# Kernel optimization log

Measured on AMD Instinct MI355X. Metric: run time of the kernel, lower is better.

## Reference

```python
import jax, jax.numpy as jnp
import numpy as np

NUM_CODES = 4096
TEMPERATURE = 1.0
EPS = 1e-08


def setup_inputs() -> dict:
    key = jax.random.key(0)
    k1, k2, k3 = jax.random.split(key, 3)
    B, D, T = 16, 512, 1500
    encoder_stride = 320
    student_features = jax.random.normal(k1, (B, D, T), dtype=jnp.float32)
    codebook = jax.random.normal(k2, (NUM_CODES, D), dtype=jnp.float32)
    lengths = jax.random.randint(k3, (B,), 0, T * encoder_stride, dtype=jnp.int64)
    return {
        "student_features": student_features,
        "codebook": codebook,
        "lengths": lengths,
        "encoder_stride": encoder_stride,
    }


def _length_mask(lengths, T, stride):
    # frame t is valid iff t < floor(length / stride)  -> (B, T) float mask
    n_valid = jnp.minimum(lengths // stride, T)
    return (jnp.arange(T)[None, :] < n_valid[:, None]).astype(jnp.float32)


def reference(student_features, codebook, lengths, encoder_stride):
    B, D, T = student_features.shape
    mask = _length_mask(lengths, T, encoder_stride)            # (B, T)
    z = jnp.transpose(student_features, (0, 2, 1)).reshape(-1, D)  # (N, D), N = B*T
    # Euclidean cdist via ||z||^2 + ||c||^2 - 2 z c^T (same as torch.cdist GEMM path)
    z2 = jnp.sum(z * z, axis=-1, keepdims=True)                # (N, 1)
    c2 = jnp.sum(codebook * codebook, axis=-1)                 # (K,)
    d2 = z2 + c2[None, :] - 2.0 * (z @ codebook.T)             # (N, K)
    distances = jnp.sqrt(jnp.maximum(d2, 1e-12))
    logits = -distances / TEMPERATURE
    probs = jax.nn.softmax(logits, axis=-1)                    # (N, K)
    probs_masked = probs * mask.reshape(-1, 1)
    code_dist = jnp.sum(probs_masked, axis=0)                  # (K,)
    code_dist = code_dist / (jnp.sum(code_dist) + EPS)
    entropy = -jnp.sum(code_dist * jnp.log(code_dist + EPS))
    max_entropy = jnp.log(jnp.float32(NUM_CODES))
    return 1.0 - entropy / max_entropy
```

## Files before the change

### kernel.cpp

```cpp
#include <hip/hip_runtime.h>
#include <hip/hip_bf16.h>

#define NUM_B   16
#define DIM     512
#define TT      1500
#define NROWS   (NUM_B * TT)
#define NCODES  4096
#define ROW_TILES ((NROWS + 127) / 128)
#define NROWS_PAD (ROW_TILES * 128)
#define NSLICE  8
#define SHIFTC  30.0f
#define NBLKX   (NCODES / 128)
#define TBLKS   (NUM_B * 47)
#define CBLKS   (NCODES / 4)
#define NZERO   (NROWS_PAD + NSLICE * NCODES)
#define NZERO2  (NZERO + 1)

typedef __bf16 bf16x8 __attribute__((ext_vector_type(8)));
typedef float  floatx4 __attribute__((ext_vector_type(4)));
typedef unsigned short ushortx8 __attribute__((ext_vector_type(8)));

__device__ __forceinline__ void glds16(const void* g, void* l) {
    __builtin_amdgcn_global_load_lds(
        (__attribute__((address_space(1))) void*)(void*)g,
        (__attribute__((address_space(3))) void*)l, 16, 0, 0);
}

__global__ __launch_bounds__(256) void k_prep(
    const float* __restrict__ sf, const float* __restrict__ cb,
    unsigned short* __restrict__ zbf, unsigned short* __restrict__ cbbf,
    float* __restrict__ z2, float* __restrict__ c2, float* __restrict__ zero0,
    float* __restrict__ outp) {
    int id = blockIdx.x, tid = threadIdx.x;
    if (id < TBLKS) {
        __shared__ float tile[32][257];
        int b = id / 47, t0 = (id % 47) * 32;
        int tl = tid & 31, dg = tid >> 5;
        int tr = tid >> 3, dgr = tid & 7;
        int tg = t0 + tr;
        float ssq = 0.f;
        unsigned short* dst = zbf + (size_t)(b * TT + tg) * DIM;
#pragma unroll
        for (int half = 0; half < 2; ++half) {
            int dbase = half * 256;
            if (half) __syncthreads();
            int t = t0 + tl;
            if (t < TT) {
                const float* src = sf + (size_t)(b * DIM + dbase + dg * 32) * TT + t;
#pragma unroll
                for (int k = 0; k < 32; ++k)
                    tile[tl][dg * 32 + k] = src[(size_t)k * TT];
            }
            __syncthreads();
            if (tg < TT) {
#pragma unroll
                for (int seg = 0; seg < 4; ++seg) {
                    int d0 = seg * 64 + dgr * 8;
                    unsigned int h[8];
#pragma unroll
                    for (int i2 = 0; i2 < 8; ++i2) {
                        __hip_bfloat16 hb = __float2bfloat16(tile[tr][d0 + i2]);
                        h[i2] = __builtin_bit_cast(unsigned short, hb);
                        float vb = __bfloat162float(hb);
                        ssq += vb * vb;
                    }
                    uint4 o;
                    o.x = h[0] | (h[1] << 16); o.y = h[2] | (h[3] << 16);
                    o.z = h[4] | (h[5] << 16); o.w = h[6] | (h[7] << 16);
                    *(uint4*)(dst + dbase + d0) = o;
                }
            }
        }
        ssq += __shfl_xor(ssq, 1); ssq += __shfl_xor(ssq, 2); ssq += __shfl_xor(ssq, 4);
        if (dgr == 0 && tg < TT) z2[b * TT + tg] = ssq;
    } else {
        int ci = id - TBLKS;
        int gid = ci * 256 + tid;
        if (gid < NZERO2) zero0[gid] = 0.f;
        if (ci == 0 && tid == 0) outp[0] = 1.0f;
        int k = ci * 4 + (tid >> 6);
        int lane = tid & 63;
        const float4* src = (const float4*)(cb + (size_t)k * DIM + lane * 8);
        float4 a = src[0], b2 = src[1];
        float vals[8] = {a.x, a.y, a.z, a.w, b2.x, b2.y, b2.z, b2.w};
        float s = 0.f;
        unsigned int h[8];
#pragma unroll
        for (int i = 0; i < 8; ++i) {
            __hip_bfloat16 hb = __float2bfloat16(vals[i]);
            h[i] = __builtin_bit_cast(unsigned short, hb);
            float vb = __bfloat162float(hb);
            s += vb * vb;
        }
        uint4 o;
        o.x = h[0] | (h[1] << 16); o.y = h[2] | (h[3] << 16);
        o.z = h[4] | (h[5] << 16); o.w = h[6] | (h[7] << 16);
        *(uint4*)(cbbf + (size_t)k * DIM + lane * 8) = o;
#pragma unroll
        for (int off = 32; off >= 1; off >>= 1) s += __shfl_down(s, off);
        if (lane == 0) c2[k] = s;
    }
}

__global__ __launch_bounds__(256, 2) void k_gemm1(
    const unsigned short* __restrict__ zbf, const unsigned short* __restrict__ cbbf,
    const float* __restrict__ z2, const float* __restrict__ c2,
    const int* __restrict__ lengths, const int* __restrict__ stride_p,
    float* __restrict__ Sg, unsigned short* __restrict__ Eg) {
    __shared__ unsigned short As[128 * 64];
    __shared__ unsigned short Bs[128 * 64];
    __shared__ float z2s[128], c2s[128];
    __shared__ unsigned char vldp[128];
    __shared__ int s_any;
    int tid = threadIdx.x;
    int r0 = blockIdx.y * 128, c0 = blockIdx.x * 128;
    if (tid == 0) s_any = 0;
    __syncthreads();
    if (tid < 128) {
        int n = r0 + tid;
        int valid = 0;
        if (n < NROWS) {
            int b = n / TT, t = n - b * TT;
            int stride = stride_p[0];
            int nv = lengths[b] / stride;
            if (nv > TT) nv = TT;
            valid = (t < nv);
        }
        if (valid) atomicOr(&s_any, 1);
        vldp[tid] = (unsigned char)valid;
        z2s[tid] = z2[r0 + tid];
        c2s[tid] = c2[c0 + tid];
    }
    __syncthreads();
    if (!s_any) return;

    int wave = tid >> 6, lane = tid & 63;
    int l15 = lane & 15, l4 = lane >> 4;
    int wr = (wave >> 1) * 64, wc = (wave & 1) * 64;

    int srow = lane >> 3;
    int scg = (lane & 7) ^ srow;
    const unsigned short* ag = zbf + (size_t)(r0 + wave * 32 + srow) * DIM + scg * 8;
    const unsigned short* bg = cbbf + (size_t)(c0 + wave * 32 + srow) * DIM + scg * 8;
    unsigned short* al = As + (wave * 32) * 64;
    unsigned short* bl = Bs + (wave * 32) * 64;

    floatx4 acc[4][4];
    const floatx4 zero = {0.f, 0.f, 0.f, 0.f};
#pragma unroll
    for (int i = 0; i < 4; ++i)
#pragma unroll
        for (int j = 0; j < 4; ++j) acc[i][j] = zero;

    int sw = l15 & 7;

    for (int kc = 0; kc < 8; ++kc) {
#pragma unroll
        for (int q = 0; q < 4; ++q) {
            glds16(ag + (size_t)q * 8 * DIM + kc * 64, al + q * 8 * 64);
            glds16(bg + (size_t)q * 8 * DIM + kc * 64, bl + q * 8 * 64);
        }
        __syncthreads();
#pragma unroll
        for (int ks = 0; ks < 64; ks += 32) {
            int g = (ks >> 3) + l4;
            int pcg = g ^ sw;
            bf16x8 av[4], bv[4];
#pragma unroll
            for (int i = 0; i < 4; ++i)
                av[i] = __builtin_bit_cast(bf16x8,
                    *(const ushortx8*)&As[(wr + 16 * i + l15) * 64 + pcg * 8]);
#pragma unroll
            for (int j = 0; j < 4; ++j)
                bv[j] = __builtin_bit_cast(bf16x8,
                    *(const ushortx8*)&Bs[(wc + 16 * j + l15) * 64 + pcg * 8]);
#pragma unroll
            for (int i = 0; i < 4; ++i)
#pragma unroll
                for (int j = 0; j < 4; ++j)
                    acc[i][j] = __builtin_amdgcn_mfma_f32_16x16x32_bf16(bv[j], av[i], acc[i][j], 0, 0, 0);
        }
        __syncthreads();
    }

    float c2r[4][4];
#pragma unroll
    for (int j = 0; j < 4; ++j)
#pragma unroll
        for (int r = 0; r < 4; ++r)
            c2r[j][r] = c2s[wc + 16 * j + 4 * l4 + r];

#pragma unroll
    for (int i = 0; i < 4; ++i) {
        int rl = wr + 16 * i + l15;
        bool rv = vldp[rl] != 0;
        float z2v = z2s[rl];
        float s = 0.f;
        unsigned short* Ep = Eg + (size_t)(r0 + rl) * NCODES + c0 + wc + l4 * 4;
#pragma unroll
        for (int j = 0; j < 4; ++j) {
            float e[4];
#pragma unroll
            for (int r = 0; r < 4; ++r) {
                float d2 = z2v + c2r[j][r] - 2.0f * acc[i][j][r];
                float d = sqrtf(fmaxf(d2, 1e-12f));
                e[r] = __expf(SHIFTC - d);
                s += e[r];
            }
            if (rv) {
                unsigned h0 = __builtin_bit_cast(unsigned short, __float2bfloat16(e[0]));
                unsigned h1 = __builtin_bit_cast(unsigned short, __float2bfloat16(e[1]));
                unsigned h2 = __builtin_bit_cast(unsigned short, __float2bfloat16(e[2]));
                unsigned h3 = __builtin_bit_cast(unsigned short, __float2bfloat16(e[3]));
                uint2 o;
                o.x = h0 | (h1 << 16);
                o.y = h2 | (h3 << 16);
                *(uint2*)(Ep + 16 * j) = o;
            }
        }
        s += __shfl_xor(s, 16); s += __shfl_xor(s, 32);
        if (l4 == 0 && rv) atomicAdd(&Sg[r0 + rl], s);
    }
}

__global__ __launch_bounds__(256) void k_scan(
    const unsigned short* __restrict__ Eg, const float* __restrict__ Sg,
    const int* __restrict__ lengths, const int* __restrict__ stride_p,
    float* __restrict__ cdp) {
    __shared__ float rs2[64];
    __shared__ unsigned char vrows[64];
    __shared__ int s_cnt;
    int tid = threadIdx.x;
    int r0 = blockIdx.y * 64;
    if (tid < 64) {
        int valid = 0;
        float inv = 0.f;
        int n = r0 + tid;
        if (n < NROWS) {
            int b = n / TT, t = n - b * TT;
            int nv = lengths[b] / stride_p[0];
            if (nv > TT) nv = TT;
            valid = (t < nv);
            if (valid) inv = 1.0f / Sg[n];
        }
        unsigned long long mask = __ballot(valid);
        if (tid == 0) s_cnt = __popcll(mask);
        if (valid) {
            int pos = __popcll(mask & ((1ull << tid) - 1ull));
            vrows[pos] = (unsigned char)tid;
            rs2[pos] = inv;
        }
    }
    __syncthreads();
    int m = s_cnt;
    if (m == 0) return;

    int col0 = blockIdx.x * 2048 + tid * 8;
    const unsigned short* base = Eg + (size_t)r0 * NCODES + col0;
    float acc[8] = {0.f, 0.f, 0.f, 0.f, 0.f, 0.f, 0.f, 0.f};

#define ACC8(V, RN) do { \
    unsigned int _u[4] = {(V).x, (V).y, (V).z, (V).w}; \
    _Pragma("unroll") \
    for (int q = 0; q < 4; ++q) { \
        acc[2 * q]     += (RN) * __builtin_bit_cast(float, _u[q] << 16); \
        acc[2 * q + 1] += (RN) * __builtin_bit_cast(float, _u[q] & 0xffff0000u); \
    } \
} while (0)

    int i = 0;
    for (; i + 8 <= m; i += 8) {
        uint4 v0 = *(const uint4*)(base + (size_t)vrows[i]     * NCODES);
        uint4 v1 = *(const uint4*)(base + (size_t)vrows[i + 1] * NCODES);
        uint4 v2 = *(const uint4*)(base + (size_t)vrows[i + 2] * NCODES);
        uint4 v3 = *(const uint4*)(base + (size_t)vrows[i + 3] * NCODES);
        uint4 v4 = *(const uint4*)(base + (size_t)vrows[i + 4] * NCODES);
        uint4 v5 = *(const uint4*)(base + (size_t)vrows[i + 5] * NCODES);
        uint4 v6 = *(const uint4*)(base + (size_t)vrows[i + 6] * NCODES);
        uint4 v7 = *(const uint4*)(base + (size_t)vrows[i + 7] * NCODES);
        ACC8(v0, rs2[i]);     ACC8(v1, rs2[i + 1]);
        ACC8(v2, rs2[i + 2]); ACC8(v3, rs2[i + 3]);
        ACC8(v4, rs2[i + 4]); ACC8(v5, rs2[i + 5]);
        ACC8(v6, rs2[i + 6]); ACC8(v7, rs2[i + 7]);
    }
    for (; i < m; ++i) {
        uint4 v = *(const uint4*)(base + (size_t)vrows[i] * NCODES);
        ACC8(v, rs2[i]);
    }
#undef ACC8

    float* outp = cdp + (size_t)(blockIdx.y & (NSLICE - 1)) * NCODES;
#pragma unroll
    for (int t = 0; t < 8; ++t) atomicAdd(&outp[col0 + t], acc[t]);
}

template <int PASS>
__global__ __launch_bounds__(256, 2) void k_gemm(
    const unsigned short* __restrict__ zbf, const unsigned short* __restrict__ cbbf,
    const float* __restrict__ z2, const float* __restrict__ c2,
    const int* __restrict__ lengths, const int* __restrict__ stride_p,
    float* __restrict__ Sg, float* __restrict__ cd) {
    __shared__ unsigned short Asf[128 * 64];
    __shared__ unsigned short Bsf[128 * 64];
    __shared__ float z2s[128], c2s[128], rs[128];
    __shared__ int s_any;
    int tid = threadIdx.x;
    int r0 = blockIdx.y * 128, c0 = blockIdx.x * 128;
    if (tid == 0) s_any = 0;
    __syncthreads();
    if (tid < 128) {
        int n = r0 + tid;
        int valid = 0;
        if (n < NROWS) {
            int b = n / TT, t = n - b * TT;
            int stride = stride_p[0];
            int nv = lengths[b] / stride;
            if (nv > TT) nv = TT;
            valid = (t < nv);
        }
        if (valid) atomicOr(&s_any, 1);
        z2s[tid] = z2[r0 + tid];
        c2s[tid] = c2[c0 + tid];
        if (PASS == 2) rs[tid] = valid ? (1.0f / Sg[r0 + tid]) : 0.0f;
    }
    __syncthreads();
    if (!s_any) return;

    int wave = tid >> 6, lane = tid & 63;
    int l15 = lane & 15, l4 = lane >> 4;
    int wr = (wave >> 1) * 64, wc = (wave & 1) * 64;
    int srow = lane >> 3;
    int scg = (lane & 7) ^ srow;
    const unsigned short* ag = zbf + (size_t)(r0 + wave * 32 + srow) * DIM + scg * 8;
    const unsigned short* bg = cbbf + (size_t)(c0 + wave * 32 + srow) * DIM + scg * 8;
    unsigned short* al = Asf + (wave * 32) * 64;
    unsigned short* bl = Bsf + (wave * 32) * 64;

    floatx4 acc[4][4];
    const floatx4 zero = {0.f, 0.f, 0.f, 0.f};
#pragma unroll
    for (int i = 0; i < 4; ++i)
#pragma unroll
        for (int j = 0; j < 4; ++j) acc[i][j] = zero;
    int sw = l15 & 7;
    for (int kc = 0; kc < 8; ++kc) {
#pragma unroll
        for (int q = 0; q < 4; ++q) {
            glds16(ag + (size_t)q * 8 * DIM + kc * 64, al + q * 8 * 64);
            glds16(bg + (size_t)q * 8 * DIM + kc * 64, bl + q * 8 * 64);
        }
        __syncthreads();
#pragma unroll
        for (int ks = 0; ks < 64; ks += 32) {
            int g = (ks >> 3) + l4;
            int pcg = g ^ sw;
            bf16x8 av[4], bvv[4];
#pragma unroll
            for (int i = 0; i < 4; ++i)
                av[i] = __builtin_bit_cast(bf16x8, *(const ushortx8*)&Asf[(wr + 16 * i + l15) * 64 + pcg * 8]);
#pragma unroll
            for (int j = 0; j < 4; ++j)
                bvv[j] = __builtin_bit_cast(bf16x8, *(const ushortx8*)&Bsf[(wc + 16 * j + l15) * 64 + pcg * 8]);
#pragma unroll
            for (int i = 0; i < 4; ++i)
#pragma unroll
                for (int j = 0; j < 4; ++j)
                    acc[i][j] = __builtin_amdgcn_mfma_f32_16x16x32_bf16(av[i], bvv[j], acc[i][j], 0, 0, 0);
        }
        __syncthreads();
    }
    if (PASS == 1) {
#pragma unroll
        for (int i = 0; i < 4; ++i) {
#pragma unroll
            for (int r = 0; r < 4; ++r) {
                int rl = wr + 16 * i + 4 * l4 + r;
                float z2v = z2s[rl];
                float s = 0.f;
#pragma unroll
                for (int j = 0; j < 4; ++j) {
                    int cl = wc + 16 * j + l15;
                    float d2 = z2v + c2s[cl] - 2.0f * acc[i][j][r];
                    float d = sqrtf(fmaxf(d2, 1e-12f));
                    s += __expf(SHIFTC - d);
                }
                s += __shfl_xor(s, 1); s += __shfl_xor(s, 2);
                s += __shfl_xor(s, 4); s += __shfl_xor(s, 8);
                if (l15 == 0) atomicAdd(&Sg[r0 + rl], s);
            }
        }
    } else {
#pragma unroll
        for (int j = 0; j < 4; ++j) {
            int cl = wc + 16 * j + l15;
            float c2v = c2s[cl];
            float cs = 0.f;
#pragma unroll
            for (int i = 0; i < 4; ++i) {
#pragma unroll
                for (int r = 0; r < 4; ++r) {
                    int rl = wr + 16 * i + 4 * l4 + r;
                    float d2 = z2s[rl] + c2v - 2.0f * acc[i][j][r];
                    float d = sqrtf(fmaxf(d2, 1e-12f));
                    cs += __expf(SHIFTC - d) * rs[rl];
                }
            }
            cs += __shfl_xor(cs, 16); cs += __shfl_xor(cs, 32);
            if (l4 == 0) atomicAdd(&cd[c0 + cl], cs);
        }
    }
}

__global__ __launch_bounds__(256) void k_red(float* __restrict__ cdp,
                                             float* __restrict__ tot) {
    int k = blockIdx.x * 256 + threadIdx.x;
    float v = 0.f;
#pragma unroll
    for (int s = 0; s < NSLICE; ++s) v += cdp[(size_t)s * NCODES + k];
    cdp[k] = v;
    float t = v;
#pragma unroll
    for (int off = 32; off >= 1; off >>= 1) t += __shfl_down(t, off);
    if ((threadIdx.x & 63) == 0) atomicAdd(tot, t);
}

__global__ __launch_bounds__(256) void k_ent(const float* __restrict__ cdp,
                                             const float* __restrict__ tot,
                                             float* __restrict__ out) {
    int k = blockIdx.x * 256 + threadIdx.x;
    float inv = 1.0f / (tot[0] + 1e-8f);
    float p = cdp[k] * inv;
    float e = p * __logf(p + 1e-8f);
#pragma unroll
    for (int off = 32; off >= 1; off >>= 1) e += __shfl_down(e, off);
    if ((threadIdx.x & 63) == 0)
        atomicAdd(out, e * (1.0f / __logf((float)NCODES)));
}

extern "C" void kernel_launch(void* const* d_in, const int* in_sizes, int n_in,
                              void* d_out, int out_size, void* d_ws, size_t ws_size,
                              hipStream_t stream) {
    const float* sf = (const float*)d_in[0];
    const float* cb = (const float*)d_in[1];
    const int* lengths = (const int*)d_in[2];
    const int* stride_p = (const int*)d_in[3];

    float* wsf = (float*)d_ws;
    float* Sg = wsf;
    float* cdp = Sg + NROWS_PAD;
    float* tot = wsf + NZERO;
    const size_t OFF_Z2 = NZERO2;
    const size_t OFF_C2 = OFF_Z2 + NROWS_PAD;
    const size_t OFF_ZB = (OFF_C2 + NCODES + 3) & ~(size_t)3;
    float* z2 = wsf + OFF_Z2;
    float* c2 = wsf + OFF_C2;
    unsigned short* zbf = (unsigned short*)(wsf + OFF_ZB);
    unsigned short* cbbf = zbf + (size_t)NROWS_PAD * DIM;
    unsigned short* Eg = cbbf + (size_t)NCODES * DIM;

    size_t need = OFF_ZB * 4
                + ((size_t)NROWS_PAD * DIM + (size_t)NCODES * DIM
                 + (size_t)NROWS_PAD * NCODES) * 2;

    k_prep<<<dim3(TBLKS + CBLKS), 256, 0, stream>>>(
        sf, cb, zbf, cbbf, z2, c2, Sg, (float*)d_out);
    if (ws_size >= need) {
        k_gemm1<<<dim3(NBLKX, ROW_TILES), 256, 0, stream>>>(
            zbf, cbbf, z2, c2, lengths, stride_p, Sg, Eg);
        k_scan<<<dim3(2, NROWS_PAD / 64), 256, 0, stream>>>(
            Eg, Sg, lengths, stride_p, cdp);
    } else {
        k_gemm<1><<<dim3(NBLKX, ROW_TILES), 256, 0, stream>>>(zbf, cbbf, z2, c2, lengths, stride_p, Sg, cdp);
        k_gemm<2><<<dim3(NBLKX, ROW_TILES), 256, 0, stream>>>(zbf, cbbf, z2, c2, lengths, stride_p, Sg, cdp);
    }
    k_red<<<dim3(NCODES / 256), 256, 0, stream>>>(cdp, tot);
    k_ent<<<dim3(NCODES / 256), 256, 0, stream>>>(cdp, tot, (float*)d_out);
}
```

Before: 224.1 us.

## Rewrite distance GEMM as 256x256 eight-wave tile with double-buffered LDS ping-pong

The k_gemm1 tile grows from 128x128 with 4 waves to 256x256 with 8 waves. LDS is double-buffered so global-to-LDS loads for tile t+2 are issued while tile t is being computed. Inline ds_read_b128 calls, explicit s_barrier/waitcnt scheduling and s_setprio around the MFMA bursts are meant to interleave LDS reads with matrix math and raise data reuse per loaded byte. In exchange there are more registers (a 8x4 accumulator), fewer blocks for load balancing, and extra prefetches past K on the last iterations that read beyond the row into the adjacent workspace.

```diff
diff --git a/kernel.cpp b/kernel.cpp
--- a/kernel.cpp
+++ b/kernel.cpp
@@ -16,6 +16,10 @@
 #define NZERO   (NROWS_PAD + NSLICE * NCODES)
 #define NZERO2  (NZERO + 1)
 
+#define NTY2 (NROWS_PAD / 256)
+#define NTX2 (NCODES / 256)
+#define KTILES (DIM / 64)
+
 typedef __bf16 bf16x8 __attribute__((ext_vector_type(8)));
 typedef float  floatx4 __attribute__((ext_vector_type(4)));
 typedef unsigned short ushortx8 __attribute__((ext_vector_type(8)));
@@ -102,29 +106,69 @@
     }
 }
 
-__global__ __launch_bounds__(256, 2) void k_gemm1(
+
+#define DSR(dst, addr) asm volatile("ds_read_b128 %0, %1" : "=v"(dst) : "v"(addr))
+#define BARR() asm volatile("s_barrier" ::: "memory")
+#define WAIT_LGKM() do { \
+    asm volatile("s_waitcnt lgkmcnt(0)" ::: "memory"); \
+    __builtin_amdgcn_sched_barrier(0); \
+} while (0)
+#define VMC8() asm volatile("s_waitcnt vmcnt(8)" ::: "memory")
+
+#define STG_A(TT_, H_) do { \
+    const unsigned short* _s = agp + (size_t)(H_) * 128 * DIM + (TT_) * 64; \
+    unsigned short* _d = &As[(TT_) & 1][H_][0] + (wave << 9); \
+    glds16(_s, _d); glds16(_s + (size_t)64 * DIM, _d + 4096); \
+} while (0)
+#define STG_B(TT_, H_) do { \
+    const unsigned short* _s = bgp + (size_t)(H_) * 128 * DIM + (TT_) * 64; \
+    unsigned short* _d = &Bs[(TT_) & 1][H_][0] + (wave << 9); \
+    glds16(_s, _d); glds16(_s + (size_t)64 * DIM, _d + 4096); \
+} while (0)
+
+#define MFMA16(IB, BV, JB) do { \
+    __builtin_amdgcn_s_setprio(1); \
+    _Pragma("unroll") \
+    for (int ii = 0; ii < 4; ++ii) { \
+        _Pragma("unroll") \
+        for (int jj = 0; jj < 2; ++jj) { \
+            floatx4 c_ = acc[(IB) + ii][(JB) + jj]; \
+            c_ = __builtin_amdgcn_mfma_f32_16x16x32_bf16( \
+                __builtin_bit_cast(bf16x8, BV[jj][0]), \
+                __builtin_bit_cast(bf16x8, av[(IB) + ii][0]), c_, 0, 0, 0); \
+            c_ = __builtin_amdgcn_mfma_f32_16x16x32_bf16( \
+                __builtin_bit_cast(bf16x8, BV[jj][1]), \
+                __builtin_bit_cast(bf16x8, av[(IB) + ii][1]), c_, 0, 0, 0); \
+            acc[(IB) + ii][(JB) + jj] = c_; \
+        } \
+    } \
+    __builtin_amdgcn_s_setprio(0); \
+} while (0)
+
+__global__ __launch_bounds__(512) void k_gemm1(
     const unsigned short* __restrict__ zbf, const unsigned short* __restrict__ cbbf,
     const float* __restrict__ z2, const float* __restrict__ c2,
     const int* __restrict__ lengths, const int* __restrict__ stride_p,
     float* __restrict__ Sg, unsigned short* __restrict__ Eg) {
-    __shared__ unsigned short As[128 * 64];
-    __shared__ unsigned short Bs[128 * 64];
-    __shared__ float z2s[128], c2s[128];
-    __shared__ unsigned char vldp[128];
+    __shared__ alignas(16) unsigned short As[2][2][8192];
+    __shared__ alignas(16) unsigned short Bs[2][2][8192];
+    __shared__ float z2s[256], c2s[256];
+    __shared__ unsigned char vldp[256];
     __shared__ int s_any;
+
     int tid = threadIdx.x;
-    int r0 = blockIdx.y * 128, c0 = blockIdx.x * 128;
+    int r0 = blockIdx.y * 256, c0 = blockIdx.x * 256;
+
     if (tid == 0) s_any = 0;
     __syncthreads();
-    if (tid < 128) {
+    if (tid < 256) {
         int n = r0 + tid;
         int valid = 0;
         if (n < NROWS) {
-            int b = n / TT, t = n - b * TT;
-            int stride = stride_p[0];
-            int nv = lengths[b] / stride;
+            int b = n / TT, t_ = n - b * TT;
+            int nv = lengths[b] / stride_p[0];
             if (nv > TT) nv = TT;
-            valid = (t < nv);
+            valid = (t_ < nv);
         }
         if (valid) atomicOr(&s_any, 1);
         vldp[tid] = (unsigned char)valid;
@@ -136,51 +180,73 @@
 
     int wave = tid >> 6, lane = tid & 63;
     int l15 = lane & 15, l4 = lane >> 4;
-    int wr = (wave >> 1) * 64, wc = (wave & 1) * 64;
-
-    int srow = lane >> 3;
-    int scg = (lane & 7) ^ srow;
-    const unsigned short* ag = zbf + (size_t)(r0 + wave * 32 + srow) * DIM + scg * 8;
-    const unsigned short* bg = cbbf + (size_t)(c0 + wave * 32 + srow) * DIM + scg * 8;
-    unsigned short* al = As + (wave * 32) * 64;
-    unsigned short* bl = Bs + (wave * 32) * 64;
-
-    floatx4 acc[4][4];
-    const floatx4 zero = {0.f, 0.f, 0.f, 0.f};
-#pragma unroll
-    for (int i = 0; i < 4; ++i)
-#pragma unroll
-        for (int j = 0; j < 4; ++j) acc[i][j] = zero;
-
-    int sw = l15 & 7;
-
-    for (int kc = 0; kc < 8; ++kc) {
-#pragma unroll
-        for (int q = 0; q < 4; ++q) {
-            glds16(ag + (size_t)q * 8 * DIM + kc * 64, al + q * 8 * 64);
-            glds16(bg + (size_t)q * 8 * DIM + kc * 64, bl + q * 8 * 64);
-        }
-        __syncthreads();
-#pragma unroll
-        for (int ks = 0; ks < 64; ks += 32) {
-            int g = (ks >> 3) + l4;
-            int pcg = g ^ sw;
-            bf16x8 av[4], bv[4];
-#pragma unroll
-            for (int i = 0; i < 4; ++i)
-                av[i] = __builtin_bit_cast(bf16x8,
-                    *(const ushortx8*)&As[(wr + 16 * i + l15) * 64 + pcg * 8]);
-#pragma unroll
-            for (int j = 0; j < 4; ++j)
-                bv[j] = __builtin_bit_cast(bf16x8,
-                    *(const ushortx8*)&Bs[(wc + 16 * j + l15) * 64 + pcg * 8]);
-#pragma unroll
-            for (int i = 0; i < 4; ++i)
-#pragma unroll
-                for (int j = 0; j < 4; ++j)
-                    acc[i][j] = __builtin_amdgcn_mfma_f32_16x16x32_bf16(bv[j], av[i], acc[i][j], 0, 0, 0);
-        }
-        __syncthreads();
+    int wr2 = wave >> 2;
+    int wc4 = wave & 3;
+
+    int srow8 = lane >> 3;
+    int sg = (lane & 7) ^ srow8;
+    const unsigned short* agp = zbf + (size_t)(r0 + wave * 8 + srow8) * DIM + sg * 8;
+    const unsigned short* bgp = cbbf + (size_t)(c0 + wave * 8 + srow8) * DIM + sg * 8;
+
+    unsigned AsB = (unsigned)(size_t)&As[0][0][0] + (unsigned)(wr2 * 16384);
+    unsigned BsB = (unsigned)(size_t)&Bs[0][0][0] + (unsigned)((wc4 >> 1) * 16384);
+    unsigned rowA = (unsigned)(l15 * 128);
+    unsigned rowB = (unsigned)(((wc4 & 1) * 64 + l15) * 128);
+    unsigned p0 = (unsigned)(((l4) ^ (l15 & 7)) * 16);
+    unsigned p1 = (unsigned)(((4 + l4) ^ (l15 & 7)) * 16);
+
+    floatx4 acc[8][4];
+    const floatx4 zacc = {0.f, 0.f, 0.f, 0.f};
+#pragma unroll
+    for (int i = 0; i < 8; ++i)
+#pragma unroll
+        for (int j = 0; j < 4; ++j) acc[i][j] = zacc;
+
+    STG_B(0, 0); STG_B(0, 1); STG_A(0, 0); STG_A(0, 1);
+    STG_B(1, 0); STG_B(1, 1); STG_A(1, 0); STG_A(1, 1);
+    VMC8();
+    BARR();
+
+    ushortx8 av[8][2];
+    ushortx8 bv01[2][2];
+    ushortx8 bv23[2][2];
+
+#pragma unroll
+    for (int t = 0; t < KTILES; ++t) {
+        unsigned dbase = (unsigned)((t & 1) * 32768);
+        unsigned aA = AsB + dbase + rowA;
+        unsigned aB = BsB + dbase + rowB;
+
+        DSR(av[0][0], aA + p0); DSR(av[1][0], aA + 2048u + p0);
+        DSR(av[2][0], aA + 4096u + p0); DSR(av[3][0], aA + 6144u + p0);
+        DSR(av[0][1], aA + p1); DSR(av[1][1], aA + 2048u + p1);
+        DSR(av[2][1], aA + 4096u + p1); DSR(av[3][1], aA + 6144u + p1);
+        DSR(bv01[0][0], aB + p0); DSR(bv01[1][0], aB + 2048u + p0);
+        DSR(bv01[0][1], aB + p1); DSR(bv01[1][1], aB + 2048u + p1);
+        BARR(); WAIT_LGKM();
+        MFMA16(0, bv01, 0);
+        BARR();
+
+        DSR(bv23[0][0], aB + 4096u + p0); DSR(bv23[1][0], aB + 6144u + p0);
+        DSR(bv23[0][1], aB + 4096u + p1); DSR(bv23[1][1], aB + 6144u + p1);
+        BARR(); WAIT_LGKM();
+        MFMA16(0, bv23, 2);
+        BARR();
+
+        DSR(av[4][0], aA + 8192u + p0); DSR(av[5][0], aA + 10240u + p0);
+        DSR(av[6][0], aA + 12288u + p0); DSR(av[7][0], aA + 14336u + p0);
+        DSR(av[4][1], aA + 8192u + p1); DSR(av[5][1], aA + 10240u + p1);
+        DSR(av[6][1], aA + 12288u + p1); DSR(av[7][1], aA + 14336u + p1);
+        STG_B(t + 2, 0); STG_B(t + 2, 1);
+        BARR(); WAIT_LGKM();
+        MFMA16(4, bv01, 0);
+        BARR();
+
+        STG_A(t + 2, 0); STG_A(t + 2, 1);
+        VMC8();
+        BARR();
+        MFMA16(4, bv23, 2);
+        BARR();
     }
 
     float c2r[4][4];
@@ -188,15 +254,15 @@
     for (int j = 0; j < 4; ++j)
 #pragma unroll
         for (int r = 0; r < 4; ++r)
-            c2r[j][r] = c2s[wc + 16 * j + 4 * l4 + r];
-
-#pragma unroll
-    for (int i = 0; i < 4; ++i) {
-        int rl = wr + 16 * i + l15;
+            c2r[j][r] = c2s[wc4 * 64 + j * 16 + l4 * 4 + r];
+
+#pragma unroll
+    for (int i = 0; i < 8; ++i) {
+        int rl = wr2 * 128 + i * 16 + l15;
         bool rv = vldp[rl] != 0;
         float z2v = z2s[rl];
         float s = 0.f;
-        unsigned short* Ep = Eg + (size_t)(r0 + rl) * NCODES + c0 + wc + l4 * 4;
+        unsigned short* Ep = Eg + (size_t)(r0 + rl) * NCODES + c0 + wc4 * 64 + l4 * 4;
 #pragma unroll
         for (int j = 0; j < 4; ++j) {
             float e[4];
@@ -465,7 +531,7 @@
     k_prep<<<dim3(TBLKS + CBLKS), 256, 0, stream>>>(
         sf, cb, zbf, cbbf, z2, c2, Sg, (float*)d_out);
     if (ws_size >= need) {
-        k_gemm1<<<dim3(NBLKX, ROW_TILES), 256, 0, stream>>>(
+        k_gemm1<<<dim3(NTX2, NTY2), 512, 0, stream>>>(
             zbf, cbbf, z2, c2, lengths, stride_p, Sg, Eg);
         k_scan<<<dim3(2, NROWS_PAD / 64), 256, 0, stream>>>(
             Eg, Sg, lengths, stride_p, cdp);
```

Measured after the change: 257.1 us. +14.7%, slower.

## Fuse column-sum scan into gemm1 via last-arriving block per row tile

Applied to the files above, without the earlier changes.

Removes the separate k_scan launch. Each gemm1 block increments a per-row-tile counter after writing its exp tile, and the last block of the tile sums the bf16 exp values weighted by inverse row sums into the code distribution. This removes a kernel boundary and lets the scan overlap with remaining gemm blocks. In exchange, the scan work runs on fewer, later-finishing blocks with 16 columns per thread, adding fences and a counter in the workspace.

```diff
diff --git a/kernel.cpp b/kernel.cpp
--- a/kernel.cpp
+++ b/kernel.cpp
@@ -15,6 +15,7 @@
 #define CBLKS   (NCODES / 4)
 #define NZERO   (NROWS_PAD + NSLICE * NCODES)
 #define NZERO2  (NZERO + 1)
+#define NZERO3  (NZERO2 + ROW_TILES)
 
 typedef __bf16 bf16x8 __attribute__((ext_vector_type(8)));
 typedef float  floatx4 __attribute__((ext_vector_type(4)));
@@ -76,7 +77,7 @@
     } else {
         int ci = id - TBLKS;
         int gid = ci * 256 + tid;
-        if (gid < NZERO2) zero0[gid] = 0.f;
+        if (gid < NZERO3) zero0[gid] = 0.f;
         if (ci == 0 && tid == 0) outp[0] = 1.0f;
         int k = ci * 4 + (tid >> 6);
         int lane = tid & 63;
@@ -106,12 +107,17 @@
     const unsigned short* __restrict__ zbf, const unsigned short* __restrict__ cbbf,
     const float* __restrict__ z2, const float* __restrict__ c2,
     const int* __restrict__ lengths, const int* __restrict__ stride_p,
-    float* __restrict__ Sg, unsigned short* __restrict__ Eg) {
+    float* __restrict__ Sg, unsigned short* __restrict__ Eg,
+    int* __restrict__ pcnt, float* __restrict__ cdp) {
     __shared__ unsigned short As[128 * 64];
     __shared__ unsigned short Bs[128 * 64];
     __shared__ float z2s[128], c2s[128];
     __shared__ unsigned char vldp[128];
     __shared__ int s_any;
+    __shared__ int s_old;
+    __shared__ float rsL[128];
+    __shared__ unsigned char vrL[128];
+    __shared__ int wcnt[2];
     int tid = threadIdx.x;
     int r0 = blockIdx.y * 128, c0 = blockIdx.x * 128;
     if (tid == 0) s_any = 0;
@@ -221,77 +227,77 @@
         s += __shfl_xor(s, 16); s += __shfl_xor(s, 32);
         if (l4 == 0 && rv) atomicAdd(&Sg[r0 + rl], s);
     }
-}
-
-__global__ __launch_bounds__(256) void k_scan(
-    const unsigned short* __restrict__ Eg, const float* __restrict__ Sg,
-    const int* __restrict__ lengths, const int* __restrict__ stride_p,
-    float* __restrict__ cdp) {
-    __shared__ float rs2[64];
-    __shared__ unsigned char vrows[64];
-    __shared__ int s_cnt;
-    int tid = threadIdx.x;
-    int r0 = blockIdx.y * 64;
-    if (tid < 64) {
-        int valid = 0;
-        float inv = 0.f;
+
+    __syncthreads();
+    if (tid == 0) {
+        __threadfence();
+        s_old = atomicAdd(&pcnt[blockIdx.y], 1);
+    }
+    __syncthreads();
+    if (s_old != 31) return;
+
+    __threadfence();
+    float inv = 0.f;
+    if (tid < 128) {
         int n = r0 + tid;
         if (n < NROWS) {
             int b = n / TT, t = n - b * TT;
             int nv = lengths[b] / stride_p[0];
             if (nv > TT) nv = TT;
-            valid = (t < nv);
-            if (valid) inv = 1.0f / Sg[n];
-        }
-        unsigned long long mask = __ballot(valid);
-        if (tid == 0) s_cnt = __popcll(mask);
-        if (valid) {
-            int pos = __popcll(mask & ((1ull << tid) - 1ull));
-            vrows[pos] = (unsigned char)tid;
-            rs2[pos] = inv;
-        }
-    }
-    __syncthreads();
-    int m = s_cnt;
-    if (m == 0) return;
-
-    int col0 = blockIdx.x * 2048 + tid * 8;
-    const unsigned short* base = Eg + (size_t)r0 * NCODES + col0;
-    float acc[8] = {0.f, 0.f, 0.f, 0.f, 0.f, 0.f, 0.f, 0.f};
-
-#define ACC8(V, RN) do { \
-    unsigned int _u[4] = {(V).x, (V).y, (V).z, (V).w}; \
+            if (t < nv) inv = 1.0f / Sg[n];
+        }
+    }
+    unsigned long long mb = __ballot(tid < 128 && inv != 0.f);
+    if (tid < 128 && (tid & 63) == 0) wcnt[tid >> 6] = __popcll(mb);
+    __syncthreads();
+    if (tid < 128 && inv != 0.f) {
+        int pos = __popcll(mb & ((1ull << (tid & 63)) - 1ull))
+                + ((tid >> 6) ? wcnt[0] : 0);
+        vrL[pos] = (unsigned char)tid;
+        rsL[pos] = inv;
+    }
+    __syncthreads();
+    int m = wcnt[0] + wcnt[1];
+
+    int cc = tid * 16;
+    const unsigned short* eb = Eg + (size_t)r0 * NCODES + cc;
+    float a2[16];
+#pragma unroll
+    for (int q = 0; q < 16; ++q) a2[q] = 0.f;
+
+#define ACC16(V0, V1, RN) do { \
+    unsigned int _u[8] = {(V0).x, (V0).y, (V0).z, (V0).w, \
+                          (V1).x, (V1).y, (V1).z, (V1).w}; \
     _Pragma("unroll") \
-    for (int q = 0; q < 4; ++q) { \
-        acc[2 * q]     += (RN) * __builtin_bit_cast(float, _u[q] << 16); \
-        acc[2 * q + 1] += (RN) * __builtin_bit_cast(float, _u[q] & 0xffff0000u); \
+    for (int q = 0; q < 8; ++q) { \
+        a2[2 * q]     += (RN) * __builtin_bit_cast(float, _u[q] << 16); \
+        a2[2 * q + 1] += (RN) * __builtin_bit_cast(float, _u[q] & 0xffff0000u); \
     } \
 } while (0)
 
-    int i = 0;
-    for (; i + 8 <= m; i += 8) {
-        uint4 v0 = *(const uint4*)(base + (size_t)vrows[i]     * NCODES);
-        uint4 v1 = *(const uint4*)(base + (size_t)vrows[i + 1] * NCODES);
-        uint4 v2 = *(const uint4*)(base + (size_t)vrows[i + 2] * NCODES);
-        uint4 v3 = *(const uint4*)(base + (size_t)vrows[i + 3] * NCODES);
-        uint4 v4 = *(const uint4*)(base + (size_t)vrows[i + 4] * NCODES);
-        uint4 v5 = *(const uint4*)(base + (size_t)vrows[i + 5] * NCODES);
-        uint4 v6 = *(const uint4*)(base + (size_t)vrows[i + 6] * NCODES);
-        uint4 v7 = *(const uint4*)(base + (size_t)vrows[i + 7] * NCODES);
-        ACC8(v0, rs2[i]);     ACC8(v1, rs2[i + 1]);
-        ACC8(v2, rs2[i + 2]); ACC8(v3, rs2[i + 3]);
-        ACC8(v4, rs2[i + 4]); ACC8(v5, rs2[i + 5]);
-        ACC8(v6, rs2[i + 6]); ACC8(v7, rs2[i + 7]);
-    }
-    for (; i < m; ++i) {
-        uint4 v = *(const uint4*)(base + (size_t)vrows[i] * NCODES);
-        ACC8(v, rs2[i]);
-    }
-#undef ACC8
+    int i2 = 0;
+    for (; i2 + 4 <= m; i2 += 4) {
+        const unsigned short* p0 = eb + (size_t)vrL[i2]     * NCODES;
+        const unsigned short* p1 = eb + (size_t)vrL[i2 + 1] * NCODES;
+        const unsigned short* p2 = eb + (size_t)vrL[i2 + 2] * NCODES;
+        const unsigned short* p3 = eb + (size_t)vrL[i2 + 3] * NCODES;
+        uint4 a0 = *(const uint4*)p0, b0 = *(const uint4*)(p0 + 8);
+        uint4 a1 = *(const uint4*)p1, b1 = *(const uint4*)(p1 + 8);
+        uint4 a2v = *(const uint4*)p2, b2v = *(const uint4*)(p2 + 8);
+        uint4 a3 = *(const uint4*)p3, b3 = *(const uint4*)(p3 + 8);
+        ACC16(a0, b0, rsL[i2]);     ACC16(a1, b1, rsL[i2 + 1]);
+        ACC16(a2v, b2v, rsL[i2 + 2]); ACC16(a3, b3, rsL[i2 + 3]);
+    }
+    for (; i2 < m; ++i2) {
+        const unsigned short* p0 = eb + (size_t)vrL[i2] * NCODES;
+        uint4 a0 = *(const uint4*)p0, b0 = *(const uint4*)(p0 + 8);
+        ACC16(a0, b0, rsL[i2]);
+    }
+#undef ACC16
 
     float* outp = cdp + (size_t)(blockIdx.y & (NSLICE - 1)) * NCODES;
 #pragma unroll
-    for (int t = 0; t < 8; ++t) atomicAdd(&outp[col0 + t], acc[t]);
+    for (int q = 0; q < 16; ++q) atomicAdd(&outp[cc + q], a2[q]);
 }
 
 template <int PASS>
@@ -449,7 +455,8 @@
     float* Sg = wsf;
     float* cdp = Sg + NROWS_PAD;
     float* tot = wsf + NZERO;
-    const size_t OFF_Z2 = NZERO2;
+    int* pcnt = (int*)(wsf + NZERO2);
+    const size_t OFF_Z2 = NZERO3;
     const size_t OFF_C2 = OFF_Z2 + NROWS_PAD;
     const size_t OFF_ZB = (OFF_C2 + NCODES + 3) & ~(size_t)3;
     float* z2 = wsf + OFF_Z2;
@@ -466,9 +473,7 @@
         sf, cb, zbf, cbbf, z2, c2, Sg, (float*)d_out);
     if (ws_size >= need) {
         k_gemm1<<<dim3(NBLKX, ROW_TILES), 256, 0, stream>>>(
-            zbf, cbbf, z2, c2, lengths, stride_p, Sg, Eg);
-        k_scan<<<dim3(2, NROWS_PAD / 64), 256, 0, stream>>>(
-            Eg, Sg, lengths, stride_p, cdp);
+            zbf, cbbf, z2, c2, lengths, stride_p, Sg, Eg, pcnt, cdp);
     } else {
         k_gemm<1><<<dim3(NBLKX, ROW_TILES), 256, 0, stream>>>(zbf, cbbf, z2, c2, lengths, stride_p, Sg, cdp);
         k_gemm<2><<<dim3(NBLKX, ROW_TILES), 256, 0, stream>>>(zbf, cbbf, z2, c2, lengths, stride_p, Sg, cdp);
```

After: 493.4 us. +120.1%, slower.
